# Kernel optimization log

Hardware: AMD Instinct MI355X
Metric: run time of the kernel (lower is better)

Reference implementation:

```python
import jax, jax.numpy as jnp
import numpy as np

N = 100_000   # nodes
E = 1_600_000 # edges (avg degree 16)
F_IN, H1, H2, H3, C = 32, 32, 32, 16, 8


def _gcn_conv(h, W, b, src, dst, norm):
    # h: [N, Fin] -> project then normalized sparse aggregate (PyG GCNConv)
    h = h @ W                                   # [N, Fout]
    msg = h[src] * norm[:, None]                # gather + scale, [E', Fout]
    agg = jax.ops.segment_sum(msg, dst, num_segments=N)
    return agg + b


def setup_inputs() -> dict:
    key = jax.random.key(0)
    ks = jax.random.split(key, 8)
    x = jax.random.normal(ks[0], (N, F_IN), dtype=jnp.float32)
    edge_index = jax.random.randint(ks[1], (2, E), 0, N, dtype=jnp.int64)
    def w(k, fi, fo):
        return jax.random.normal(k, (fi, fo), dtype=jnp.float32) / np.float32(np.sqrt(fi))
    return {
        "x": x,
        "edge_index": edge_index,
        "W1": w(ks[2], F_IN, H1), "b1": jnp.zeros((H1,), jnp.float32),
        "W2": w(ks[3], H1, H2),   "b2": jnp.zeros((H2,), jnp.float32),
        "W3": w(ks[4], H2, H3),   "b3": jnp.zeros((H3,), jnp.float32),
        "Wc": w(ks[5], H3, C),    "bc": jnp.zeros((C,), jnp.float32),
    }


def reference(x, edge_index, W1, b1, W2, b2, W3, b3, Wc, bc):
    src, dst = edge_index[0], edge_index[1]
    loops = jnp.arange(N, dtype=src.dtype)
    src_f = jnp.concatenate([src, loops])       # add self-loops
    dst_f = jnp.concatenate([dst, loops])
    # symmetric normalization D^-1/2 (A+I) D^-1/2 (deg over targets, incl. self-loop)
    deg = jax.ops.segment_sum(jnp.ones_like(dst_f, dtype=x.dtype), dst_f, num_segments=N)
    dinv = jax.lax.rsqrt(deg)                   # deg >= 1 due to self-loops
    norm = dinv[src_f] * dinv[dst_f]            # [E+N]

    h = jnp.tanh(_gcn_conv(x, W1, b1, src_f, dst_f, norm))
    h = jnp.tanh(_gcn_conv(h, W2, b2, src_f, dst_f, norm))
    h = jnp.tanh(_gcn_conv(h, W3, b3, src_f, dst_f, norm))
    out = h @ Wc + bc
    return (out, h)
```

## Files before the change

### kernel.cpp

```cpp
#include <hip/hip_runtime.h>
#include <hip/hip_fp16.h>

static constexpr int NN = 100000;
static constexpr int NE = 1600000;

static constexpr int BSH   = 9;
static constexpr int NDB   = 1 << BSH;
static constexpr int NBUCK = (NN + NDB - 1) / NDB;
static constexpr int BCAP  = 9216;
static constexpr int HSTRIDE = 6656;
static constexpr int BSTRIDE = 2 * HSTRIDE;
static constexpr int TILE  = 4096;
static constexpr int NBIN  = (NE + TILE - 1) / TILE;
static constexpr int EPT   = TILE / 256;

static_assert(NBUCK <= 256, "bucket count must fit one block");
static_assert(NN % 32 == 0, "grids assume divisibility");

__device__ __forceinline__ float4 h4tof4(uint2 r) {
    const __half2 a = *reinterpret_cast<const __half2*>(&r.x);
    const __half2 b = *reinterpret_cast<const __half2*>(&r.y);
    const float2 fa = __half22float2(a);
    const float2 fb = __half22float2(b);
    return make_float4(fa.x, fa.y, fb.x, fb.y);
}
__device__ __forceinline__ unsigned packh2(float a, float b) {
    __half2 h = __floats2half2_rn(a, b);
    return *reinterpret_cast<unsigned*>(&h);
}

__global__ __launch_bounds__(256) void k_bin_proj(const int* __restrict__ src,
                                                  const int* __restrict__ dst,
                                                  int* __restrict__ gcur,
                                                  unsigned* __restrict__ bkt,
                                                  const float* __restrict__ x,
                                                  const float* __restrict__ W1,
                                                  __half* __restrict__ p) {
    const int t = threadIdx.x;
    if (blockIdx.x < NBIN) {
        __shared__ int hist[NBUCK];
        __shared__ int cur[NBUCK];
        const int e0 = blockIdx.x * TILE;
        const int n = (NE - e0 < TILE) ? (NE - e0) : TILE;
        for (int i = t; i < NBUCK; i += 256) hist[i] = 0;
        __syncthreads();
        unsigned rec[EPT];
        int bb[EPT];
#pragma unroll
        for (int j = 0; j < EPT; ++j) {
            const int i = t + j * 256;
            bb[j] = -1;
            if (i < n) {
                const int s = src[e0 + i];
                const int d = dst[e0 + i];
                bb[j] = d >> BSH;
                rec[j] = ((unsigned)s << BSH) | (unsigned)(d & (NDB - 1));
                atomicAdd(&hist[bb[j]], 1);
            }
        }
        __syncthreads();
        for (int i = t; i < NBUCK; i += 256) {
            const int c = hist[i];
            cur[i] = (c > 0) ? (i * BCAP + atomicAdd(&gcur[i], c)) : 0;
        }
        __syncthreads();
#pragma unroll
        for (int j = 0; j < EPT; ++j) {
            if (bb[j] >= 0) {
                const int pos = atomicAdd(&cur[bb[j]], 1);
                bkt[pos] = rec[j];
            }
        }
    } else {
        __shared__ float Ws[1024];
        __shared__ float xr[16][33];
        const int pb = blockIdx.x - NBIN;
        if (pb == 0 && t < 16) ((unsigned*)p)[(size_t)NN * 16 + t] = 0u;
        for (int i = t; i < 1024; i += 256) Ws[i] = W1[i];
        const int nl = t >> 4;
        const int f2 = t & 15;
        const int node = pb * 16 + nl;
        const float2 xv = ((const float2*)x)[(size_t)node * 16 + f2];
        xr[nl][2 * f2] = xv.x;
        xr[nl][2 * f2 + 1] = xv.y;
        __syncthreads();
        float a0 = 0.f, a1 = 0.f;
#pragma unroll
        for (int k = 0; k < 32; ++k) {
            const float hv = xr[nl][k];
            a0 += hv * Ws[k * 32 + 2 * f2];
            a1 += hv * Ws[k * 32 + 2 * f2 + 1];
        }
        ((unsigned*)p)[(size_t)node * 16 + f2] = packh2(a0, a1);
    }
}

__global__ __launch_bounds__(256) void k_build(const unsigned* __restrict__ bkt,
                                               const int* __restrict__ gcur,
                                               int* __restrict__ csr,
                                               int* __restrict__ npad,
                                               int* __restrict__ offs,
                                               float* __restrict__ dinv,
                                               __half* __restrict__ B0) {
    __shared__ int hist[256];
    __shared__ int sc[256];
    __shared__ int cur[256];
    const int bb = blockIdx.x;
    const int b = bb >> 1;
    const unsigned half = bb & 1;
    const int h0 = (b << BSH) + (int)half * 256;
    const int nh = (NN - h0 < 256) ? (NN - h0) : 256;
    const int t = threadIdx.x;
    int cnt = gcur[b];
    if (cnt > BCAP) cnt = BCAP;
    hist[t] = 0;
    __syncthreads();
    const unsigned* bp = bkt + (size_t)b * BCAP;
    if (nh > 0) {
        for (int i = t; i < cnt; i += 256) {
            const unsigned r = bp[i];
            if (((r >> 8) & 1u) == half) atomicAdd(&hist[r & 255], 1);
        }
    }
    __syncthreads();
    const int h = hist[t];
    const int lp = (h + 7) & ~7;
    sc[t] = lp;
    __syncthreads();
    for (int off = 1; off < 256; off <<= 1) {
        const int a = (t >= off) ? sc[t - off] : 0;
        __syncthreads();
        sc[t] += a;
        __syncthreads();
    }
    const int rbase = b * BSTRIDE + (int)half * HSTRIDE;
    const int e = rbase + (sc[t] - lp);
    cur[t] = e;
    if (t < nh) {
        const int node = h0 + t;
        npad[node] = lp;
        offs[node] = e;
        dinv[node] = rsqrtf((float)h + 1.0f);
        for (int j = h; j < lp; ++j) csr[e + j] = NN;
    }
    __syncthreads();
    if (nh > 0) {
        for (int i = t; i < cnt; i += 256) {
            const unsigned r = bp[i];
            if (((r >> 8) & 1u) == half) {
                const int pos = atomicAdd(&cur[r & 255], 1);
                csr[pos] = (int)(r >> BSH);
            }
        }
        unsigned* P = (unsigned*)B0;
        for (int i = t; i < nh * 16; i += 256) {
            const int node = h0 + (i >> 4);
            const float di = dinv[node];
            unsigned v = P[(size_t)node * 16 + (i & 15)];
            float2 f = __half22float2(*reinterpret_cast<__half2*>(&v));
            P[(size_t)node * 16 + (i & 15)] = packh2(f.x * di, f.y * di);
        }
    }
}

template <int FOUT>
__global__ __launch_bounds__(256) void k_agg_proj(const uint2* __restrict__ pu,
                                                  const int* __restrict__ offs,
                                                  const int* __restrict__ npad,
                                                  const float* __restrict__ dinv,
                                                  const int* __restrict__ csr,
                                                  const float4* __restrict__ bias4,
                                                  const float* __restrict__ W,
                                                  __half* __restrict__ pout) {
    constexpr int NPB = 32;
    constexpr int OPL = FOUT / 8;
    __shared__ float Ws[32 * FOUT];
    __shared__ float hs[NPB][33];
    const int tid = threadIdx.x;
    if (blockIdx.x == 0 && tid < FOUT / 2)
        ((unsigned*)pout)[(size_t)NN * (FOUT / 2) + tid] = 0u;
    for (int i = tid; i < 32 * FOUT; i += 256) Ws[i] = W[i];
    const int nl = tid >> 3;
    const int f4 = tid & 7;
    const int node = blockIdx.x * NPB + nl;
    const int start = offs[node];
    const int L = npad[node];
    const float4 self = h4tof4(pu[(size_t)node * 8 + f4]);
    float ax = self.x, ay = self.y, az = self.z, aw = self.w;
    int kk = 0;
    for (; kk + 16 <= L; kk += 16) {
        const int* cp = csr + start + kk;
        int s[16];
#pragma unroll
        for (int j = 0; j < 16; ++j) s[j] = cp[j];
        uint2 v[16];
#pragma unroll
        for (int j = 0; j < 16; ++j) v[j] = pu[(size_t)s[j] * 8 + f4];
        float sx0 = 0.f, sy0 = 0.f, sz0 = 0.f, sw0 = 0.f;
        float sx1 = 0.f, sy1 = 0.f, sz1 = 0.f, sw1 = 0.f;
#pragma unroll
        for (int j = 0; j < 8; ++j) {
            const float4 f0 = h4tof4(v[j]);
            const float4 f1 = h4tof4(v[j + 8]);
            sx0 += f0.x; sy0 += f0.y; sz0 += f0.z; sw0 += f0.w;
            sx1 += f1.x; sy1 += f1.y; sz1 += f1.z; sw1 += f1.w;
        }
        ax += sx0 + sx1; ay += sy0 + sy1; az += sz0 + sz1; aw += sw0 + sw1;
    }
    if (kk < L) {
        const int* cp = csr + start + kk;
        int s[8];
#pragma unroll
        for (int j = 0; j < 8; ++j) s[j] = cp[j];
        uint2 v[8];
#pragma unroll
        for (int j = 0; j < 8; ++j) v[j] = pu[(size_t)s[j] * 8 + f4];
#pragma unroll
        for (int j = 0; j < 8; ++j) {
            const float4 f0 = h4tof4(v[j]);
            ax += f0.x; ay += f0.y; az += f0.z; aw += f0.w;
        }
    }
    const float di = dinv[node];
    const float4 bb = bias4[f4];
    hs[nl][4 * f4 + 0] = tanhf(di * ax + bb.x);
    hs[nl][4 * f4 + 1] = tanhf(di * ay + bb.y);
    hs[nl][4 * f4 + 2] = tanhf(di * az + bb.z);
    hs[nl][4 * f4 + 3] = tanhf(di * aw + bb.w);
    __syncthreads();
    float acc[OPL];
#pragma unroll
    for (int o = 0; o < OPL; ++o) acc[o] = 0.f;
#pragma unroll
    for (int k = 0; k < 32; ++k) {
        const float hv = hs[nl][k];
#pragma unroll
        for (int o = 0; o < OPL; ++o) acc[o] += hv * Ws[k * FOUT + f4 * OPL + o];
    }
    if (OPL == 4) {
        uint2 r;
        r.x = packh2(acc[0] * di, acc[1] * di);
        r.y = packh2(acc[2] * di, acc[OPL - 1] * di);
        ((uint2*)pout)[(size_t)node * 8 + f4] = r;
    } else {
        ((unsigned*)pout)[(size_t)node * 8 + f4] = packh2(acc[0] * di, acc[OPL - 1] * di);
    }
}

__global__ __launch_bounds__(256) void k_agg_cls(const uint2* __restrict__ pu,
                                                 const int* __restrict__ offs,
                                                 const int* __restrict__ npad,
                                                 const float* __restrict__ dinv,
                                                 const int* __restrict__ csr,
                                                 const float4* __restrict__ bias4,
                                                 const float* __restrict__ Wc,
                                                 const float* __restrict__ bc,
                                                 float4* __restrict__ h4out,
                                                 float* __restrict__ out) {
    constexpr int NPB = 64;
    __shared__ float WcS[16 * 8];
    __shared__ float bcS[8];
    __shared__ float hs[NPB][17];
    const int tid = threadIdx.x;
    if (tid < 128) WcS[tid] = Wc[tid];
    if (tid < 8) bcS[tid] = bc[tid];
    const int nl = tid >> 2;
    const int f4 = tid & 3;
    int node = blockIdx.x * NPB + nl;
    if (node >= NN) node = NN - 1;
    const int start = offs[node];
    const int L = npad[node];
    const float4 self = h4tof4(pu[(size_t)node * 4 + f4]);
    float ax = self.x, ay = self.y, az = self.z, aw = self.w;
    int kk = 0;
    for (; kk + 16 <= L; kk += 16) {
        const int* cp = csr + start + kk;
        int s[16];
#pragma unroll
        for (int j = 0; j < 16; ++j) s[j] = cp[j];
        uint2 v[16];
#pragma unroll
        for (int j = 0; j < 16; ++j) v[j] = pu[(size_t)s[j] * 4 + f4];
        float sx0 = 0.f, sy0 = 0.f, sz0 = 0.f, sw0 = 0.f;
        float sx1 = 0.f, sy1 = 0.f, sz1 = 0.f, sw1 = 0.f;
#pragma unroll
        for (int j = 0; j < 8; ++j) {
            const float4 f0 = h4tof4(v[j]);
            const float4 f1 = h4tof4(v[j + 8]);
            sx0 += f0.x; sy0 += f0.y; sz0 += f0.z; sw0 += f0.w;
            sx1 += f1.x; sy1 += f1.y; sz1 += f1.z; sw1 += f1.w;
        }
        ax += sx0 + sx1; ay += sy0 + sy1; az += sz0 + sz1; aw += sw0 + sw1;
    }
    if (kk < L) {
        const int* cp = csr + start + kk;
        int s[8];
#pragma unroll
        for (int j = 0; j < 8; ++j) s[j] = cp[j];
        uint2 v[8];
#pragma unroll
        for (int j = 0; j < 8; ++j) v[j] = pu[(size_t)s[j] * 4 + f4];
#pragma unroll
        for (int j = 0; j < 8; ++j) {
            const float4 f0 = h4tof4(v[j]);
            ax += f0.x; ay += f0.y; az += f0.z; aw += f0.w;
        }
    }
    const float di = dinv[node];
    const float4 bb = bias4[f4];
    float4 h;
    h.x = tanhf(di * ax + bb.x);
    h.y = tanhf(di * ay + bb.y);
    h.z = tanhf(di * az + bb.z);
    h.w = tanhf(di * aw + bb.w);
    h4out[(size_t)node * 4 + f4] = h;
    hs[nl][4 * f4 + 0] = h.x;
    hs[nl][4 * f4 + 1] = h.y;
    hs[nl][4 * f4 + 2] = h.z;
    hs[nl][4 * f4 + 3] = h.w;
    __syncthreads();
    float a0 = bcS[2 * f4], a1 = bcS[2 * f4 + 1];
#pragma unroll
    for (int k = 0; k < 16; ++k) {
        const float hv = hs[nl][k];
        a0 += hv * WcS[k * 8 + 2 * f4];
        a1 += hv * WcS[k * 8 + 2 * f4 + 1];
    }
    reinterpret_cast<float2*>(out)[(size_t)node * 4 + f4] = make_float2(a0, a1);
}


extern "C" void kernel_launch(void* const* d_in, const int* in_sizes, int n_in,
                              void* d_out, int out_size, void* d_ws, size_t ws_size,
                              hipStream_t stream) {
    const float* x  = (const float*)d_in[0];
    const int*   ei = (const int*)d_in[1];
    const float* W1 = (const float*)d_in[2];
    const float* b1 = (const float*)d_in[3];
    const float* W2 = (const float*)d_in[4];
    const float* b2 = (const float*)d_in[5];
    const float* W3 = (const float*)d_in[6];
    const float* b3 = (const float*)d_in[7];
    const float* Wc = (const float*)d_in[8];
    const float* bc = (const float*)d_in[9];

    const int* src = ei;
    const int* dst = ei + NE;

    int*    gcur = (int*)d_ws;
    int*    npad = gcur + 256;
    int*    offs = npad + NN;
    float*  dinv = (float*)(offs + NN);
    int*    csr  = (int*)(dinv + NN);
    __half* B0   = (__half*)(csr + (size_t)NBUCK * BSTRIDE);
    __half* B1   = B0 + (size_t)(NN + 1) * 32;
    unsigned* bkt = (unsigned*)(B1 + (size_t)(NN + 1) * 32);

    float* out = (float*)d_out;
    float* h3  = out + (size_t)NN * 8;

    const int T = 256;

    hipMemsetAsync(gcur, 0, NBUCK * sizeof(int), stream);

    k_bin_proj<<<NBIN + NN / 16, T, 0, stream>>>(src, dst, gcur, bkt, x, W1, B0);

    k_build<<<2 * NBUCK, T, 0, stream>>>(bkt, gcur, csr, npad, offs, dinv, B0);

    k_agg_proj<32><<<NN / 32, T, 0, stream>>>((const uint2*)B0, offs, npad, dinv, csr,
                                              (const float4*)b1, W2, B1);

    k_agg_proj<16><<<NN / 32, T, 0, stream>>>((const uint2*)B1, offs, npad, dinv, csr,
                                              (const float4*)b2, W3, B0);

    k_agg_cls<<<(NN + 63) / 64, T, 0, stream>>>((const uint2*)B0, offs, npad, dinv, csr,
                                                (const float4*)b3, Wc, bc,
                                                (float4*)h3, out);
}
```

Baseline: 134.5 us.

## Sort nodes by padded degree within each half-bucket and vectorize CSR index loads

k_build now counting-sorts each 256-node half-bucket by padded degree (in units of 8) into a permutation array. The aggregation kernels walk nodes through this permutation, so nodes with similar neighbour counts land in the same wavefront and divergent loop trip counts are reduced. The CSR index loads are also changed to int4 vector loads, which relies on per-node offsets being padded to multiples of 8. The cost is an extra indirection and scattered node writes, plus a small amount of extra work in the build kernel.

```diff
diff --git a/kernel.cpp b/kernel.cpp
--- a/kernel.cpp
+++ b/kernel.cpp
@@ -101,10 +101,13 @@
                                                int* __restrict__ npad,
                                                int* __restrict__ offs,
                                                float* __restrict__ dinv,
+                                               int* __restrict__ perm,
                                                __half* __restrict__ B0) {
     __shared__ int hist[256];
     __shared__ int sc[256];
     __shared__ int cur[256];
+    __shared__ int dcnt[64];
+    __shared__ int dcur[64];
     const int bb = blockIdx.x;
     const int b = bb >> 1;
     const unsigned half = bb & 1;
@@ -114,6 +117,7 @@
     int cnt = gcur[b];
     if (cnt > BCAP) cnt = BCAP;
     hist[t] = 0;
+    if (t < 64) dcnt[t] = 0;
     __syncthreads();
     const unsigned* bp = bkt + (size_t)b * BCAP;
     if (nh > 0) {
@@ -161,6 +165,23 @@
             P[(size_t)node * 16 + (i & 15)] = packh2(f.x * di, f.y * di);
         }
     }
+    const int key = (t < nh) ? ((lp >> 3) < 63 ? (lp >> 3) : 63) : -1;
+    if (key >= 0) atomicAdd(&dcnt[key], 1);
+    __syncthreads();
+    if (t < 64) sc[t] = dcnt[t];
+    __syncthreads();
+    for (int off = 1; off < 64; off <<= 1) {
+        const int a = (t >= off && t < 64) ? sc[t - off] : 0;
+        __syncthreads();
+        if (t < 64) sc[t] += a;
+        __syncthreads();
+    }
+    if (t < 64) dcur[t] = sc[t] - dcnt[t];
+    __syncthreads();
+    if (key >= 0) {
+        const int pos = atomicAdd(&dcur[key], 1);
+        perm[h0 + pos] = h0 + t;
+    }
 }
 
 template <int FOUT>
@@ -169,6 +190,7 @@
                                                   const int* __restrict__ npad,
                                                   const float* __restrict__ dinv,
                                                   const int* __restrict__ csr,
+                                                  const int* __restrict__ perm,
                                                   const float4* __restrict__ bias4,
                                                   const float* __restrict__ W,
                                                   __half* __restrict__ pout) {
@@ -182,17 +204,18 @@
     for (int i = tid; i < 32 * FOUT; i += 256) Ws[i] = W[i];
     const int nl = tid >> 3;
     const int f4 = tid & 7;
-    const int node = blockIdx.x * NPB + nl;
+    const int node = perm[blockIdx.x * NPB + nl];
     const int start = offs[node];
     const int L = npad[node];
     const float4 self = h4tof4(pu[(size_t)node * 8 + f4]);
     float ax = self.x, ay = self.y, az = self.z, aw = self.w;
     int kk = 0;
     for (; kk + 16 <= L; kk += 16) {
-        const int* cp = csr + start + kk;
-        int s[16];
-#pragma unroll
-        for (int j = 0; j < 16; ++j) s[j] = cp[j];
+        const int4* cp4 = reinterpret_cast<const int4*>(csr + start + kk);
+        int4 s4[4];
+#pragma unroll
+        for (int j = 0; j < 4; ++j) s4[j] = cp4[j];
+        const int* s = reinterpret_cast<const int*>(s4);
         uint2 v[16];
 #pragma unroll
         for (int j = 0; j < 16; ++j) v[j] = pu[(size_t)s[j] * 8 + f4];
@@ -208,10 +231,10 @@
         ax += sx0 + sx1; ay += sy0 + sy1; az += sz0 + sz1; aw += sw0 + sw1;
     }
     if (kk < L) {
-        const int* cp = csr + start + kk;
-        int s[8];
-#pragma unroll
-        for (int j = 0; j < 8; ++j) s[j] = cp[j];
+        const int4* cp4 = reinterpret_cast<const int4*>(csr + start + kk);
+        int4 s4[2];
+        s4[0] = cp4[0]; s4[1] = cp4[1];
+        const int* s = reinterpret_cast<const int*>(s4);
         uint2 v[8];
 #pragma unroll
         for (int j = 0; j < 8; ++j) v[j] = pu[(size_t)s[j] * 8 + f4];
@@ -252,6 +275,7 @@
                                                  const int* __restrict__ npad,
                                                  const float* __restrict__ dinv,
                                                  const int* __restrict__ csr,
+                                                 const int* __restrict__ perm,
                                                  const float4* __restrict__ bias4,
                                                  const float* __restrict__ Wc,
                                                  const float* __restrict__ bc,
@@ -266,18 +290,20 @@
     if (tid < 8) bcS[tid] = bc[tid];
     const int nl = tid >> 2;
     const int f4 = tid & 3;
-    int node = blockIdx.x * NPB + nl;
-    if (node >= NN) node = NN - 1;
+    int slot = blockIdx.x * NPB + nl;
+    if (slot >= NN) slot = NN - 1;
+    const int node = perm[slot];
     const int start = offs[node];
     const int L = npad[node];
     const float4 self = h4tof4(pu[(size_t)node * 4 + f4]);
     float ax = self.x, ay = self.y, az = self.z, aw = self.w;
     int kk = 0;
     for (; kk + 16 <= L; kk += 16) {
-        const int* cp = csr + start + kk;
-        int s[16];
-#pragma unroll
-        for (int j = 0; j < 16; ++j) s[j] = cp[j];
+        const int4* cp4 = reinterpret_cast<const int4*>(csr + start + kk);
+        int4 s4[4];
+#pragma unroll
+        for (int j = 0; j < 4; ++j) s4[j] = cp4[j];
+        const int* s = reinterpret_cast<const int*>(s4);
         uint2 v[16];
 #pragma unroll
         for (int j = 0; j < 16; ++j) v[j] = pu[(size_t)s[j] * 4 + f4];
@@ -293,10 +319,10 @@
         ax += sx0 + sx1; ay += sy0 + sy1; az += sz0 + sz1; aw += sw0 + sw1;
     }
     if (kk < L) {
-        const int* cp = csr + start + kk;
-        int s[8];
-#pragma unroll
-        for (int j = 0; j < 8; ++j) s[j] = cp[j];
+        const int4* cp4 = reinterpret_cast<const int4*>(csr + start + kk);
+        int4 s4[2];
+        s4[0] = cp4[0]; s4[1] = cp4[1];
+        const int* s = reinterpret_cast<const int*>(s4);
         uint2 v[8];
 #pragma unroll
         for (int j = 0; j < 8; ++j) v[j] = pu[(size_t)s[j] * 4 + f4];
@@ -351,7 +377,8 @@
     int*    npad = gcur + 256;
     int*    offs = npad + NN;
     float*  dinv = (float*)(offs + NN);
-    int*    csr  = (int*)(dinv + NN);
+    int*    perm = (int*)(dinv + NN);
+    int*    csr  = perm + NN;
     __half* B0   = (__half*)(csr + (size_t)NBUCK * BSTRIDE);
     __half* B1   = B0 + (size_t)(NN + 1) * 32;
     unsigned* bkt = (unsigned*)(B1 + (size_t)(NN + 1) * 32);
@@ -365,15 +392,15 @@
 
     k_bin_proj<<<NBIN + NN / 16, T, 0, stream>>>(src, dst, gcur, bkt, x, W1, B0);
 
-    k_build<<<2 * NBUCK, T, 0, stream>>>(bkt, gcur, csr, npad, offs, dinv, B0);
+    k_build<<<2 * NBUCK, T, 0, stream>>>(bkt, gcur, csr, npad, offs, dinv, perm, B0);
 
     k_agg_proj<32><<<NN / 32, T, 0, stream>>>((const uint2*)B0, offs, npad, dinv, csr,
-                                              (const float4*)b1, W2, B1);
+                                              perm, (const float4*)b1, W2, B1);
 
     k_agg_proj<16><<<NN / 32, T, 0, stream>>>((const uint2*)B1, offs, npad, dinv, csr,
-                                              (const float4*)b2, W3, B0);
+                                              perm, (const float4*)b2, W3, B0);
 
     k_agg_cls<<<(NN + 63) / 64, T, 0, stream>>>((const uint2*)B0, offs, npad, dinv, csr,
-                                                (const float4*)b3, Wc, bc,
+                                                perm, (const float4*)b3, Wc, bc,
                                                 (float4*)h3, out);
 }
```

Measured after the change: 142.7 us. 1.06x slower.
